# Kernel optimization log

Hardware: AMD Instinct MI355X
Metric: run time of the kernel (lower is better)

Reference implementation:

```python
import jax, jax.numpy as jnp
import numpy as np


def _weighted_combine(emb, w):
    # emb: [B, L, D], w: [B, L] -> [B, D]
    sw = jnp.sum(w, axis=1, keepdims=True)          # [B, 1]
    wn = (w / sw)[..., None]                         # [B, L, 1]
    return jnp.sum(emb * wn, axis=1)


def setup_inputs() -> dict:
    key = jax.random.key(0)
    k1, k2, k3, k4, k5, k6 = jax.random.split(key, 6)
    B, La, Lb, V, D = 16384, 50, 20, 100000, 64
    return {
        "ids_single": jax.random.randint(k1, (B,), 0, V, dtype=jnp.int32),
        "ids_multi_a": jax.random.randint(k2, (B, La), 0, V, dtype=jnp.int32),
        "ids_multi_b": jax.random.randint(k3, (B, Lb), 0, V, dtype=jnp.int32),
        "weights_a": jax.random.uniform(k4, (B, La), dtype=jnp.float32),
        "weights_b": jax.random.uniform(k5, (B, Lb), dtype=jnp.float32),
        "embedding_table": jax.random.normal(k6, (V, D), dtype=jnp.float32),
    }


def reference(ids_single, ids_multi_a, ids_multi_b, weights_a, weights_b, embedding_table):
    # Per-field gather (equivalent to the flat gather + split in the original)
    e_single = embedding_table[ids_single]        # [B, D]
    e_a = embedding_table[ids_multi_a]            # [B, La, D]
    e_b = embedding_table[ids_multi_b]            # [B, Lb, D]
    # 'weight' combiner: normalize weights per row and sum-pool
    p_a = _weighted_combine(e_a, weights_a)       # [B, D]
    p_b = _weighted_combine(e_b, weights_b)       # [B, D]
    # concat along feature dim (do_concat=True)
    return jnp.concatenate([e_single, p_a, p_b], axis=-1)  # [B, 3*D]
```

## Files before the change

kernel.cpp:

```cpp
#include <hip/hip_runtime.h>

#define BATCH 16384
#define LA 50
#define LB 20
#define DIM 64

__global__ __launch_bounds__(256) void emb_pool_kernel(
    const int*   __restrict__ ids_single,
    const int*   __restrict__ ids_a,
    const int*   __restrict__ ids_b,
    const float* __restrict__ wa,
    const float* __restrict__ wb,
    const float* __restrict__ table,
    float*       __restrict__ out)
{
    const int wave = __builtin_amdgcn_readfirstlane((int)(threadIdx.x >> 6));
    const int lane = (int)(threadIdx.x & 63);
    const int b    = (int)blockIdx.x * 4 + wave;
    if (b >= BATCH) return;

    float* orow = out + (size_t)b * (3 * DIM);

    {
        const int idx = ids_single[b];
        orow[lane] = table[(size_t)idx * DIM + lane];
    }

    {
        const int*   ia = ids_a + (size_t)b * LA;
        const float* wp = wa    + (size_t)b * LA;
        float acc = 0.0f, sw = 0.0f;
#pragma unroll
        for (int l = 0; l < LA; ++l) {
            const float w   = wp[l];
            const int   idx = ia[l];
            sw  += w;
            acc += w * table[(size_t)idx * DIM + lane];
        }
        orow[DIM + lane] = acc / sw;
    }

    {
        const int*   ib = ids_b + (size_t)b * LB;
        const float* wp = wb    + (size_t)b * LB;
        float acc = 0.0f, sw = 0.0f;
#pragma unroll
        for (int l = 0; l < LB; ++l) {
            const float w   = wp[l];
            const int   idx = ib[l];
            sw  += w;
            acc += w * table[(size_t)idx * DIM + lane];
        }
        orow[2 * DIM + lane] = acc / sw;
    }
}

extern "C" void kernel_launch(void* const* d_in, const int* in_sizes, int n_in,
                              void* d_out, int out_size, void* d_ws, size_t ws_size,
                              hipStream_t stream) {
    const int*   ids_single = (const int*)  d_in[0];
    const int*   ids_a      = (const int*)  d_in[1];
    const int*   ids_b      = (const int*)  d_in[2];
    const float* wa         = (const float*)d_in[3];
    const float* wb         = (const float*)d_in[4];
    const float* table      = (const float*)d_in[5];
    float*       out        = (float*)d_out;

    const int grid = BATCH / 4;
    emb_pool_kernel<<<grid, 256, 0, stream>>>(ids_single, ids_a, ids_b,
                                              wa, wb, table, out);
}
```

Measured before the change: 119.3 us.

## Split each wave into four row groups with float4 gathers and shuffle reduction

Each 64-lane wave now handles four embedding rows at a time: lanes split into four groups of 16, and each lane loads a float4 of one row. Partial sums are combined with xor shuffles and only the first group writes a float4 result. The goal is to cut the serial gather chain per wave by four and use wider memory transactions. It adds shuffle work and select logic, and the lane groups handle the tail of 50 and 20 ids with masking.

```diff
diff --git a/kernel.cpp b/kernel.cpp
--- a/kernel.cpp
+++ b/kernel.cpp
@@ -4,6 +4,55 @@
 #define LA 50
 #define LB 20
 #define DIM 64
+
+__device__ __forceinline__ float4 ld4(const float* p) { return *(const float4*)p; }
+
+template <int L>
+__device__ __forceinline__ void pool_field(const int* __restrict__ ids,
+                                           const float* __restrict__ w,
+                                           const float* __restrict__ table,
+                                           int q, int j,
+                                           float* __restrict__ oseg) {
+    float4 acc = make_float4(0.f, 0.f, 0.f, 0.f);
+    float sw = 0.f;
+#pragma unroll
+    for (int l = 0; l < L; l += 4) {
+        int idx;
+        float wq;
+        if (l + 3 < L) {
+            const int   i0 = ids[l], i1 = ids[l + 1], i2 = ids[l + 2], i3 = ids[l + 3];
+            const float w0 = w[l],   w1 = w[l + 1],   w2 = w[l + 2],   w3 = w[l + 3];
+            sw += w0 + w1 + w2 + w3;
+            idx = (q == 0) ? i0 : (q == 1) ? i1 : (q == 2) ? i2 : i3;
+            wq  = (q == 0) ? w0 : (q == 1) ? w1 : (q == 2) ? w2 : w3;
+        } else {
+            const int   i0 = ids[l], i1 = ids[l + 1];
+            const float w0 = w[l],   w1 = w[l + 1];
+            sw += w0 + w1;
+            idx = (q & 1) ? i1 : i0;
+            wq  = (q & 1) ? w1 : w0;
+            if (q >= 2) wq = 0.f;
+        }
+        const float4 r = ld4(table + (size_t)idx * DIM + j * 4);
+        acc.x += wq * r.x;
+        acc.y += wq * r.y;
+        acc.z += wq * r.z;
+        acc.w += wq * r.w;
+    }
+#pragma unroll
+    for (int m = 16; m <= 32; m <<= 1) {
+        acc.x += __shfl_xor(acc.x, m);
+        acc.y += __shfl_xor(acc.y, m);
+        acc.z += __shfl_xor(acc.z, m);
+        acc.w += __shfl_xor(acc.w, m);
+    }
+    const float inv = 1.0f / sw;
+    if (q == 0) {
+        float4 o;
+        o.x = acc.x * inv; o.y = acc.y * inv; o.z = acc.z * inv; o.w = acc.w * inv;
+        *(float4*)(oseg + j * 4) = o;
+    }
+}
 
 __global__ __launch_bounds__(256) void emb_pool_kernel(
     const int*   __restrict__ ids_single,
@@ -16,43 +65,23 @@
 {
     const int wave = __builtin_amdgcn_readfirstlane((int)(threadIdx.x >> 6));
     const int lane = (int)(threadIdx.x & 63);
+    const int q    = lane >> 4;
+    const int j    = lane & 15;
     const int b    = (int)blockIdx.x * 4 + wave;
-    if (b >= BATCH) return;
 
     float* orow = out + (size_t)b * (3 * DIM);
 
     {
         const int idx = ids_single[b];
-        orow[lane] = table[(size_t)idx * DIM + lane];
+        const float4 r = ld4(table + (size_t)idx * DIM + j * 4);
+        if (q == 0) *(float4*)(orow + j * 4) = r;
     }
 
-    {
-        const int*   ia = ids_a + (size_t)b * LA;
-        const float* wp = wa    + (size_t)b * LA;
-        float acc = 0.0f, sw = 0.0f;
-#pragma unroll
-        for (int l = 0; l < LA; ++l) {
-            const float w   = wp[l];
-            const int   idx = ia[l];
-            sw  += w;
-            acc += w * table[(size_t)idx * DIM + lane];
-        }
-        orow[DIM + lane] = acc / sw;
-    }
+    pool_field<LA>(ids_a + (size_t)b * LA, wa + (size_t)b * LA, table, q, j,
+                   orow + DIM);
 
-    {
-        const int*   ib = ids_b + (size_t)b * LB;
-        const float* wp = wb    + (size_t)b * LB;
-        float acc = 0.0f, sw = 0.0f;
-#pragma unroll
-        for (int l = 0; l < LB; ++l) {
-            const float w   = wp[l];
-            const int   idx = ib[l];
-            sw  += w;
-            acc += w * table[(size_t)idx * DIM + lane];
-        }
-        orow[2 * DIM + lane] = acc / sw;
-    }
+    pool_field<LB>(ids_b + (size_t)b * LB, wb + (size_t)b * LB, table, q, j,
+                   orow + 2 * DIM);
 }
 
 extern "C" void kernel_launch(void* const* d_in, const int* in_sizes, int n_in,
@@ -66,7 +95,6 @@
     const float* table      = (const float*)d_in[5];
     float*       out        = (float*)d_out;
 
-    const int grid = BATCH / 4;
-    emb_pool_kernel<<<grid, 256, 0, stream>>>(ids_single, ids_a, ids_b,
-                                              wa, wb, table, out);
+    emb_pool_kernel<<<BATCH / 4, 256, 0, stream>>>(ids_single, ids_a, ids_b,
+                                                   wa, wb, table, out);
 }
```

Result: no change. 119.8 us (+0.4%).

## Gather embedding rows with float4 loads split across quarter-waves and cross-lane reduce

Applied to the files above, without the earlier changes.

Each wave now loads all ids and weights for its row in one coalesced pass, reduces the weight sums with shuffles, and broadcasts ids to quarter-waves. Each 16-lane group then fetches whole table rows as float4 loads, four rows per instruction, issuing all 13+5+1 gathers up front before accumulating. Partial sums are combined with xor-shuffles and only the first quarter-wave writes the output. This cuts the count of scalar dependent loads and raises memory-level parallelism, at the cost of more registers and 32-bit byte offsets that assume the table is under 4 GB.

```diff
diff --git a/kernel.cpp b/kernel.cpp
--- a/kernel.cpp
+++ b/kernel.cpp
@@ -4,6 +4,10 @@
 #define LA 50
 #define LB 20
 #define DIM 64
+#define NT_A 13
+#define NT_B 5
+
+__device__ __forceinline__ float4 ld4(const float* p) { return *(const float4*)p; }
 
 __global__ __launch_bounds__(256) void emb_pool_kernel(
     const int*   __restrict__ ids_single,
@@ -14,44 +18,89 @@
     const float* __restrict__ table,
     float*       __restrict__ out)
 {
-    const int wave = __builtin_amdgcn_readfirstlane((int)(threadIdx.x >> 6));
     const int lane = (int)(threadIdx.x & 63);
+    const int wave = (int)(threadIdx.x >> 6);
+    const int q    = lane >> 4;
+    const int j    = lane & 15;
     const int b    = (int)blockIdx.x * 4 + wave;
-    if (b >= BATCH) return;
 
-    float* orow = out + (size_t)b * (3 * DIM);
+    const char* tbl = (const char*)table;
+    const uint32_t jb = (uint32_t)(j << 4);
 
-    {
-        const int idx = ids_single[b];
-        orow[lane] = table[(size_t)idx * DIM + lane];
+    const int*   ia  = ids_a + (size_t)b * LA;
+    const float* wpa = wa    + (size_t)b * LA;
+    const int*   ib  = ids_b + (size_t)b * LB;
+    const float* wpb = wb    + (size_t)b * LB;
+
+    const int   aid = ia[lane < LA ? lane : LA - 1];
+    const float aw  = (lane < LA) ? wpa[lane] : 0.0f;
+    const int   bid = ib[lane < LB ? lane : LB - 1];
+    const float bw  = (lane < LB) ? wpb[lane] : 0.0f;
+    const int   sid = ids_single[b];
+
+    float swa = aw, swb = bw;
+#pragma unroll
+    for (int m = 1; m < 64; m <<= 1) {
+        swa += __shfl_xor(swa, m);
+        swb += __shfl_xor(swb, m);
+    }
+    const float inva = 1.0f / swa;
+    const float invb = 1.0f / swb;
+
+    uint32_t offA[NT_A]; float wA[NT_A];
+#pragma unroll
+    for (int t = 0; t < NT_A; ++t) {
+        const int src = 4 * t + q;
+        offA[t] = ((uint32_t)__shfl(aid, src) << 8) + jb;
+        wA[t]   = __shfl(aw, src);
+    }
+    uint32_t offB[NT_B]; float wB[NT_B];
+#pragma unroll
+    for (int t = 0; t < NT_B; ++t) {
+        const int src = 4 * t + q;
+        offB[t] = ((uint32_t)__shfl(bid, src) << 8) + jb;
+        wB[t]   = __shfl(bw, src);
+    }
+    const uint32_t offS = ((uint32_t)sid << 8) + jb;
+
+    float4 rA[NT_A];
+#pragma unroll
+    for (int t = 0; t < NT_A; ++t) rA[t] = ld4((const float*)(tbl + offA[t]));
+    float4 rB[NT_B];
+#pragma unroll
+    for (int t = 0; t < NT_B; ++t) rB[t] = ld4((const float*)(tbl + offB[t]));
+    const float4 rS = ld4((const float*)(tbl + offS));
+
+    float4 accA = make_float4(0.f, 0.f, 0.f, 0.f);
+#pragma unroll
+    for (int t = 0; t < NT_A; ++t) {
+        accA.x += wA[t] * rA[t].x; accA.y += wA[t] * rA[t].y;
+        accA.z += wA[t] * rA[t].z; accA.w += wA[t] * rA[t].w;
+    }
+    float4 accB = make_float4(0.f, 0.f, 0.f, 0.f);
+#pragma unroll
+    for (int t = 0; t < NT_B; ++t) {
+        accB.x += wB[t] * rB[t].x; accB.y += wB[t] * rB[t].y;
+        accB.z += wB[t] * rB[t].z; accB.w += wB[t] * rB[t].w;
     }
 
-    {
-        const int*   ia = ids_a + (size_t)b * LA;
-        const float* wp = wa    + (size_t)b * LA;
-        float acc = 0.0f, sw = 0.0f;
 #pragma unroll
-        for (int l = 0; l < LA; ++l) {
-            const float w   = wp[l];
-            const int   idx = ia[l];
-            sw  += w;
-            acc += w * table[(size_t)idx * DIM + lane];
-        }
-        orow[DIM + lane] = acc / sw;
+    for (int m = 16; m <= 32; m <<= 1) {
+        accA.x += __shfl_xor(accA.x, m); accA.y += __shfl_xor(accA.y, m);
+        accA.z += __shfl_xor(accA.z, m); accA.w += __shfl_xor(accA.w, m);
+        accB.x += __shfl_xor(accB.x, m); accB.y += __shfl_xor(accB.y, m);
+        accB.z += __shfl_xor(accB.z, m); accB.w += __shfl_xor(accB.w, m);
     }
 
-    {
-        const int*   ib = ids_b + (size_t)b * LB;
-        const float* wp = wb    + (size_t)b * LB;
-        float acc = 0.0f, sw = 0.0f;
-#pragma unroll
-        for (int l = 0; l < LB; ++l) {
-            const float w   = wp[l];
-            const int   idx = ib[l];
-            sw  += w;
-            acc += w * table[(size_t)idx * DIM + lane];
-        }
-        orow[2 * DIM + lane] = acc / sw;
+    if (q == 0) {
+        float* orow = out + (size_t)b * (3 * DIM);
+        *(float4*)(orow + j * 4) = rS;
+        float4 oa; oa.x = accA.x * inva; oa.y = accA.y * inva;
+                   oa.z = accA.z * inva; oa.w = accA.w * inva;
+        *(float4*)(orow + DIM + j * 4) = oa;
+        float4 ob; ob.x = accB.x * invb; ob.y = accB.y * invb;
+                   ob.z = accB.z * invb; ob.w = accB.w * invb;
+        *(float4*)(orow + 2 * DIM + j * 4) = ob;
     }
 }
 
@@ -66,7 +115,6 @@
     const float* table      = (const float*)d_in[5];
     float*       out        = (float*)d_out;
 
-    const int grid = BATCH / 4;
-    emb_pool_kernel<<<grid, 256, 0, stream>>>(ids_single, ids_a, ids_b,
-                                              wa, wb, table, out);
+    emb_pool_kernel<<<BATCH / 4, 256, 0, stream>>>(ids_single, ids_a, ids_b,
+                                                   wa, wb, table, out);
 }
```

Result: no change. 119.2 us (-0.1%).
